# Kernel optimization log

Measured on AMD Instinct MI355X. Metric: run time of the kernel, lower is better.

Reference implementation:

```python
import jax, jax.numpy as jnp
import numpy as np


def _extract_patch_points(x, p):
    # x: (n, c, h, w) -> (n, c*p*p, h*w) patch feature vectors (edge-padded),
    # matching build_extended_map + build_pts_set_for_flann ordering.
    n, c, h, w = x.shape
    step = p // 2
    y = jnp.pad(x, ((0, 0), (0, 0), (step, step), (step, step)), mode='edge')
    shifts = [y[:, :, i:i + h, j:j + w] for i in range(p) for j in range(p)]
    feat = jnp.stack(shifts, axis=2)            # (n, c, p*p, h, w)
    return feat.reshape(n, c * p * p, h * w)    # (n, d, hw)


def setup_inputs() -> dict:
    key = jax.random.key(0)
    k1, k2 = jax.random.split(key)
    source_map = jax.random.normal(k1, (1, 32, 128, 128), dtype=jnp.float32)
    target_map = jax.random.normal(k2, (1, 32, 128, 128), dtype=jnp.float32)
    return {"source_map": source_map, "target_map": target_map, "patch_size": 3}


def reference(source_map, target_map, patch_size):
    n, c, sh, sw = source_map.shape
    tw = target_map.shape[3]
    pts = _extract_patch_points(target_map, patch_size)   # (n, d, Np)
    q_pts = _extract_patch_points(source_map, patch_size) # (n, d, Nq)

    def nn_one(p_feat, q_feat):
        p = p_feat.T  # (Np, d) target points
        q = q_feat.T  # (Nq, d) query points
        r_p = jnp.sum(p * p, axis=1, keepdims=True)   # (Np, 1)
        r_q = jnp.sum(q * q, axis=1, keepdims=True)   # (Nq, 1)
        mul = q @ p.T                                  # (Nq, Np)
        # Faithful to original pairwise_dist (its r_p/r_q broadcast orientation
        # requires Np == Nq, which holds here):
        dist = r_p - 2.0 * mul + r_q.T                 # (Nq, Np)
        return jnp.argmin(dist, axis=1), jnp.min(dist, axis=1)

    nn_idx, nnd = jax.vmap(nn_one)(pts, q_pts)         # (n, Nq) each
    idy = nn_idx // tw
    idx = nn_idx % tw
    nnf = jnp.stack([idy.reshape(n, sh, sw), idx.reshape(n, sh, sw)], axis=1).astype(jnp.int32)
    nnd = nnd.reshape(n, 1, sh, sw)
    return nnf, nnd
```

## Files before the change

### kernel.cpp

```cpp
#include <hip/hip_runtime.h>
#include <stdint.h>

#define NPT   16384
#define KE    64
#define ROWB  8192

typedef _Float16 f16;
typedef __attribute__((ext_vector_type(8))) _Float16 half8;
typedef __attribute__((ext_vector_type(4))) float floatx4;

#define AS1(p) ((const __attribute__((address_space(1))) uint32_t*)(p))
#define AS3(p) ((__attribute__((address_space(3))) uint32_t*)(p))

__global__ __launch_bounds__(256)
void extract_kernel(const float* __restrict__ src, const float* __restrict__ tgt,
                    f16* __restrict__ Aext, f16* __restrict__ Bext,
                    double* __restrict__ n2s, double* __restrict__ n2t) {
  __shared__ f16 bufA[256 * KE];
  __shared__ f16 bufB[256 * KE];
  const int tid = threadIdx.x;
  const int pt = blockIdx.x * 256 + tid;
  double sA = 0.0, sB = 0.0;
#pragma unroll
  for (int c = 0; c < 32; ++c) {
    float v = src[(c << 14) + pt];
    sA += (double)v * (double)v;
    f16 h = (f16)v;
    bufA[tid * KE + c] = h;
    bufA[tid * KE + 32 + c] = (f16)(v - (float)h);
    v = tgt[(c << 14) + pt];
    sB += (double)v * (double)v;
    h = (f16)v;
    bufB[tid * KE + c] = h;
    bufB[tid * KE + 32 + c] = (f16)(v - (float)h);
  }
  n2s[pt] = sA;
  n2t[pt] = sB;
  __syncthreads();
  const uint4* s4A = (const uint4*)bufA;
  const uint4* s4B = (const uint4*)bufB;
  uint4* gA = (uint4*)(Aext + (size_t)blockIdx.x * 256 * KE);
  uint4* gB = (uint4*)(Bext + (size_t)blockIdx.x * 256 * KE);
#pragma unroll
  for (int it = 0; it < 8; ++it) {
    gA[it * 256 + tid] = s4A[it * 256 + tid];
    gB[it * 256 + tid] = s4B[it * 256 + tid];
  }
}

__global__ __launch_bounds__(256)
void norm_blur_kernel(const double* __restrict__ n2s, const double* __restrict__ n2t,
                      float* __restrict__ rq, float* __restrict__ rp,
                      unsigned long long* __restrict__ best) {
  const int pt = blockIdx.x * 256 + threadIdx.x;
  const int y = pt >> 7, x = pt & 127;
  double sq = 0.0, sp_ = 0.0;
#pragma unroll
  for (int dy = -1; dy <= 1; ++dy) {
    int yy = y + dy; yy = yy < 0 ? 0 : (yy > 127 ? 127 : yy);
#pragma unroll
    for (int dx = -1; dx <= 1; ++dx) {
      int xx = x + dx; xx = xx < 0 ? 0 : (xx > 127 ? 127 : xx);
      sq  += n2s[(yy << 7) + xx];
      sp_ += n2t[(yy << 7) + xx];
    }
  }
  rq[pt] = (float)sq;
  rp[pt] = (float)sp_;
  best[pt] = 0xFFFFFFFFFFFFFFFFULL;
}

__global__ __launch_bounds__(256, 2)
void gemm_blur_argmin_kernel(const f16* __restrict__ A, const f16* __restrict__ B,
                             const float* __restrict__ rq,
                             unsigned long long* __restrict__ best) {
  __shared__ __align__(16) char smem[65536];
  f16* Ash = (f16*)smem;
  f16* Bsh = (f16*)(smem + 16384);
  float* Cf = (float*)smem;

  const int L  = blockIdx.x;
  const int st = L >> 7;
  const int r  = L & 127;
  const int bx = ((st & 15) << 3) | (r & 7);
  const int by = ((st >> 4) << 4) | (r >> 3);
  const int yq = by;
  const int vt = bx;

  const f16* Aw[3] = { A + (size_t)(yq > 0 ? yq - 1 : 0) * ROWB,
                       A + (size_t)yq * ROWB,
                       A + (size_t)(yq < 127 ? yq + 1 : 127) * ROWB };
  const f16* Bw[3] = { B + (size_t)(vt > 0 ? vt - 1 : 0) * ROWB,
                       B + (size_t)vt * ROWB,
                       B + (size_t)(vt < 127 ? vt + 1 : 127) * ROWB };

  const int t = threadIdx.x;
  const int w = t >> 6;
  const int l = t & 63;

  const int lr = l >> 3;
  const int lt = l & 7;
  const int sl = lt ^ (lr & 7);
  int rowOff[4];
#pragma unroll
  for (int ig = 0; ig < 4; ++ig)
    rowOff[ig] = (w * 32 + ig * 8 + lr) * KE + sl * 8;

  const int m16 = l & 15;
  const int q   = l >> 4;
  const int pHi = q ^ (m16 & 7);
  const int pLo = pHi ^ 4;
  const int wRow = (w & 1) * 64;
  const int wCol = (w >> 1) * 64;
  const int aHiOff = m16 * 64 + pHi * 8;
  const int aLoOff = m16 * 64 + pLo * 8;

  floatx4 acc[4][4] = {};

#pragma unroll
  for (int kw = 0; kw < 3; ++kw) {
    __syncthreads();
#pragma unroll
    for (int ig = 0; ig < 4; ++ig)
      __builtin_amdgcn_global_load_lds(AS1(Aw[kw] + rowOff[ig]),
                                       AS3(&Ash[(w * 32 + ig * 8) * 64]), 16, 0, 0);
#pragma unroll
    for (int ig = 0; ig < 4; ++ig)
      __builtin_amdgcn_global_load_lds(AS1(Bw[kw] + rowOff[ig]),
                                       AS3(&Bsh[(w * 32 + ig * 8) * 64]), 16, 0, 0);
    __syncthreads();

    half8 ah[4], al[4];
#pragma unroll
    for (int i = 0; i < 4; ++i) {
      ah[i] = *(const half8*)&Ash[(wRow + i * 16) * 64 + aHiOff];
      al[i] = *(const half8*)&Ash[(wRow + i * 16) * 64 + aLoOff];
    }
#pragma unroll
    for (int j = 0; j < 4; ++j) {
      half8 bh = *(const half8*)&Bsh[(wCol + j * 16) * 64 + aHiOff];
#pragma unroll
      for (int i = 0; i < 4; ++i)
        acc[i][j] = __builtin_amdgcn_mfma_f32_16x16x32_f16(ah[i], bh, acc[i][j], 0, 0, 0);
#pragma unroll
      for (int i = 0; i < 4; ++i)
        acc[i][j] = __builtin_amdgcn_mfma_f32_16x16x32_f16(al[i], bh, acc[i][j], 0, 0, 0);
    }
#pragma unroll
    for (int j = 0; j < 4; ++j) {
      half8 bl = *(const half8*)&Bsh[(wCol + j * 16) * 64 + aLoOff];
#pragma unroll
      for (int i = 0; i < 4; ++i)
        acc[i][j] = __builtin_amdgcn_mfma_f32_16x16x32_f16(ah[i], bl, acc[i][j], 0, 0, 0);
    }
  }

  __syncthreads();
#pragma unroll
  for (int i = 0; i < 4; ++i) {
#pragma unroll
    for (int j = 0; j < 4; ++j) {
      const int col = wCol + j * 16 + m16;
      const int gc = col >> 2, cl = col & 3;
#pragma unroll
      for (int r2 = 0; r2 < 4; ++r2) {
        const int rr = wRow + i * 16 + q * 4 + r2;
        Cf[(rr << 7) + (((gc ^ (rr & 7)) << 2) | cl)] = acc[i][j][r2];
      }
    }
  }
  __syncthreads();

  const int xr = t >> 1;
  const int uh = t & 1;
  const int g0 = uh << 4;
  const int xm = xr > 0 ? xr - 1 : 0;
  const int xp = xr < 127 ? xr + 1 : 127;

  const floatx4* rq4 = (const floatx4*)(rq + (vt << 7));

#define LDCF(x, g) (*(const floatx4*)&Cf[((x) << 7) + ((((g) ^ ((x) & 7))) << 2)])

  unsigned long long pk = 0xFFFFFFFFFFFFFFFFULL;
  float am_last = (uh == 0) ? LDCF(xm, 0)[0] : LDCF(xm, 15)[3];
  floatx4 Ap = LDCF(xp, g0);
#pragma unroll
  for (int k = 0; k < 16; ++k) {
    const int g = g0 + k;
    const floatx4 Am = LDCF(xm, g);
    const floatx4 Ac = LDCF(xr, g);
    floatx4 ApN = Ap;
    float ap4;
    if (g < 31) { ApN = LDCF(xp, g + 1); ap4 = ApN[0]; }
    else        { ap4 = Ap[3]; }
    const floatx4 rv = rq4[g];
    float o[4];
    o[0] = am_last + Ac[0] + Ap[1];
    o[1] = Am[0]   + Ac[1] + Ap[2];
    o[2] = Am[1]   + Ac[2] + Ap[3];
    o[3] = Am[2]   + Ac[3] + ap4;
    am_last = Am[3];
    Ap = ApN;
    const int colb = (vt << 7) + (g << 2);
#pragma unroll
    for (int e = 0; e < 4; ++e) {
      float f = fmaf(-2.0f, o[e], rv[e]);
      unsigned int bits = __float_as_uint(f);
      unsigned int key = (bits & 0x80000000u) ? ~bits : (bits | 0x80000000u);
      unsigned long long cand =
          ((unsigned long long)key << 32) | (unsigned)(colb + e);
      pk = pk < cand ? pk : cand;
    }
  }
  unsigned long long ov = __shfl_xor(pk, 1);
  pk = pk < ov ? pk : ov;
  if (uh == 0) atomicMin(best + (yq << 7) + xr, pk);
}

__global__ void finalize_kernel(const unsigned long long* __restrict__ best,
                                const float* __restrict__ rp,
                                float* __restrict__ out) {
  int i = blockIdx.x * 256 + threadIdx.x;
  if (i >= NPT) return;
  unsigned long long v = best[i];
  unsigned int col = (unsigned int)(v & 0xFFFFFFFFu);
  unsigned int key = (unsigned int)(v >> 32);
  unsigned int bits = (key & 0x80000000u) ? (key & 0x7FFFFFFFu) : ~key;
  float fmin = __uint_as_float(bits);
  out[i]           = (float)(col >> 7);
  out[NPT + i]     = (float)(col & 127);
  out[2 * NPT + i] = rp[i] + fmin;
}

extern "C" void kernel_launch(void* const* d_in, const int* in_sizes, int n_in,
                              void* d_out, int out_size, void* d_ws, size_t ws_size,
                              hipStream_t stream) {
  const float* src = (const float*)d_in[0];
  const float* tgt = (const float*)d_in[1];
  float* out = (float*)d_out;

  char* ws = (char*)d_ws;
  f16* Aext = (f16*)(ws);
  f16* Bext = (f16*)(ws + 2097152);
  double* n2s = (double*)(ws + 4194304);
  double* n2t = (double*)(ws + 4325376);
  float* rq = (float*)(ws + 4456448);
  float* rp = (float*)(ws + 4521984);
  unsigned long long* best = (unsigned long long*)(ws + 4587520);

  extract_kernel<<<64, 256, 0, stream>>>(src, tgt, Aext, Bext, n2s, n2t);
  norm_blur_kernel<<<64, 256, 0, stream>>>(n2s, n2t, rq, rp, best);
  gemm_blur_argmin_kernel<<<16384, 256, 0, stream>>>(Aext, Bext, rq, best);
  finalize_kernel<<<NPT / 256, 256, 0, stream>>>(best, rp, out);
}
```

Measured before the change: 344.4 us.

## Load GEMM operands directly to registers and halve epilogue LDS for higher occupancy

The GEMM stage now loads A/B fragments straight from global memory into registers instead of staging them through LDS with global_load_lds. The epilogue writes the 128x128 C tile to a 65-row LDS buffer in two phases, with a halo row, which cuts shared memory from 64KB to about 33KB. Launch bounds are raised to 4 blocks per CU. The argmin now tracks a float/index pair instead of packed 64-bit keys, with 4 threads per row. The cost is uncoalesced direct global fragment loads and an extra barrier phase.

```diff
diff --git a/kernel.cpp b/kernel.cpp
--- a/kernel.cpp
+++ b/kernel.cpp
@@ -8,9 +8,6 @@
 typedef _Float16 f16;
 typedef __attribute__((ext_vector_type(8))) _Float16 half8;
 typedef __attribute__((ext_vector_type(4))) float floatx4;
-
-#define AS1(p) ((const __attribute__((address_space(1))) uint32_t*)(p))
-#define AS3(p) ((__attribute__((address_space(3))) uint32_t*)(p))
 
 __global__ __launch_bounds__(256)
 void extract_kernel(const float* __restrict__ src, const float* __restrict__ tgt,
@@ -70,14 +67,11 @@
   best[pt] = 0xFFFFFFFFFFFFFFFFULL;
 }
 
-__global__ __launch_bounds__(256, 2)
+__global__ __launch_bounds__(256, 4)
 void gemm_blur_argmin_kernel(const f16* __restrict__ A, const f16* __restrict__ B,
                              const float* __restrict__ rq,
                              unsigned long long* __restrict__ best) {
-  __shared__ __align__(16) char smem[65536];
-  f16* Ash = (f16*)smem;
-  f16* Bsh = (f16*)(smem + 16384);
-  float* Cf = (float*)smem;
+  __shared__ __align__(16) float Cf[65 * 128];
 
   const int L  = blockIdx.x;
   const int st = L >> 7;
@@ -97,124 +91,124 @@
   const int t = threadIdx.x;
   const int w = t >> 6;
   const int l = t & 63;
-
-  const int lr = l >> 3;
-  const int lt = l & 7;
-  const int sl = lt ^ (lr & 7);
-  int rowOff[4];
-#pragma unroll
-  for (int ig = 0; ig < 4; ++ig)
-    rowOff[ig] = (w * 32 + ig * 8 + lr) * KE + sl * 8;
-
   const int m16 = l & 15;
   const int q   = l >> 4;
-  const int pHi = q ^ (m16 & 7);
-  const int pLo = pHi ^ 4;
   const int wRow = (w & 1) * 64;
   const int wCol = (w >> 1) * 64;
-  const int aHiOff = m16 * 64 + pHi * 8;
-  const int aLoOff = m16 * 64 + pLo * 8;
+
+  int aIdx[4], bIdx[4];
+#pragma unroll
+  for (int i = 0; i < 4; ++i) aIdx[i] = (wRow + i * 16 + m16) * KE + q * 8;
+#pragma unroll
+  for (int j = 0; j < 4; ++j) bIdx[j] = (wCol + j * 16 + m16) * KE + q * 8;
 
   floatx4 acc[4][4] = {};
 
 #pragma unroll
   for (int kw = 0; kw < 3; ++kw) {
+    const f16* __restrict__ Ak = Aw[kw];
+    const f16* __restrict__ Bk = Bw[kw];
+    half8 ah[4], al[4], bh[4], bl[4];
+#pragma unroll
+    for (int i = 0; i < 4; ++i) {
+      ah[i] = *(const half8*)(Ak + aIdx[i]);
+      al[i] = *(const half8*)(Ak + aIdx[i] + 32);
+    }
+#pragma unroll
+    for (int j = 0; j < 4; ++j) {
+      bh[j] = *(const half8*)(Bk + bIdx[j]);
+      bl[j] = *(const half8*)(Bk + bIdx[j] + 32);
+    }
+#pragma unroll
+    for (int j = 0; j < 4; ++j) {
+#pragma unroll
+      for (int i = 0; i < 4; ++i)
+        acc[i][j] = __builtin_amdgcn_mfma_f32_16x16x32_f16(ah[i], bh[j], acc[i][j], 0, 0, 0);
+#pragma unroll
+      for (int i = 0; i < 4; ++i)
+        acc[i][j] = __builtin_amdgcn_mfma_f32_16x16x32_f16(al[i], bh[j], acc[i][j], 0, 0, 0);
+#pragma unroll
+      for (int i = 0; i < 4; ++i)
+        acc[i][j] = __builtin_amdgcn_mfma_f32_16x16x32_f16(ah[i], bl[j], acc[i][j], 0, 0, 0);
+    }
+  }
+
+#define SWZ(row, col) (((row) << 7) + ((((col) >> 2) ^ ((row) & 7)) << 2) + ((col) & 3))
+#define LDCF(row, g) (*(const floatx4*)&Cf[((row) << 7) + ((((g) ^ ((row) & 7))) << 2)])
+
+  const int xr_l = t >> 2;
+  const int uq = t & 3;
+  const int g0 = uq << 3;
+  const floatx4* rq4 = (const floatx4*)(rq + (vt << 7));
+
+#pragma unroll
+  for (int ph = 0; ph < 2; ++ph) {
+    if ((ph == 0) ? (wRow == 0) : (wRow == 64)) {
+      const int rbase = ph;
+#pragma unroll
+      for (int i = 0; i < 4; ++i)
+#pragma unroll
+        for (int j = 0; j < 4; ++j) {
+          const int col = wCol + j * 16 + m16;
+#pragma unroll
+          for (int r2 = 0; r2 < 4; ++r2) {
+            const int lrow = rbase + i * 16 + q * 4 + r2;
+            Cf[SWZ(lrow, col)] = acc[i][j][r2];
+          }
+        }
+    } else if ((ph == 0) ? (q == 0) : (q == 3)) {
+      const int lrow = ph ? 0 : 64;
+#pragma unroll
+      for (int j = 0; j < 4; ++j) {
+        const int col = wCol + j * 16 + m16;
+        Cf[SWZ(lrow, col)] = ph ? acc[3][j][3] : acc[0][j][0];
+      }
+    }
     __syncthreads();
-#pragma unroll
-    for (int ig = 0; ig < 4; ++ig)
-      __builtin_amdgcn_global_load_lds(AS1(Aw[kw] + rowOff[ig]),
-                                       AS3(&Ash[(w * 32 + ig * 8) * 64]), 16, 0, 0);
-#pragma unroll
-    for (int ig = 0; ig < 4; ++ig)
-      __builtin_amdgcn_global_load_lds(AS1(Bw[kw] + rowOff[ig]),
-                                       AS3(&Bsh[(w * 32 + ig * 8) * 64]), 16, 0, 0);
-    __syncthreads();
-
-    half8 ah[4], al[4];
-#pragma unroll
-    for (int i = 0; i < 4; ++i) {
-      ah[i] = *(const half8*)&Ash[(wRow + i * 16) * 64 + aHiOff];
-      al[i] = *(const half8*)&Ash[(wRow + i * 16) * 64 + aLoOff];
-    }
-#pragma unroll
-    for (int j = 0; j < 4; ++j) {
-      half8 bh = *(const half8*)&Bsh[(wCol + j * 16) * 64 + aHiOff];
-#pragma unroll
-      for (int i = 0; i < 4; ++i)
-        acc[i][j] = __builtin_amdgcn_mfma_f32_16x16x32_f16(ah[i], bh, acc[i][j], 0, 0, 0);
-#pragma unroll
-      for (int i = 0; i < 4; ++i)
-        acc[i][j] = __builtin_amdgcn_mfma_f32_16x16x32_f16(al[i], bh, acc[i][j], 0, 0, 0);
-    }
-#pragma unroll
-    for (int j = 0; j < 4; ++j) {
-      half8 bl = *(const half8*)&Bsh[(wCol + j * 16) * 64 + aLoOff];
-#pragma unroll
-      for (int i = 0; i < 4; ++i)
-        acc[i][j] = __builtin_amdgcn_mfma_f32_16x16x32_f16(ah[i], bl, acc[i][j], 0, 0, 0);
-    }
-  }
-
-  __syncthreads();
-#pragma unroll
-  for (int i = 0; i < 4; ++i) {
-#pragma unroll
-    for (int j = 0; j < 4; ++j) {
-      const int col = wCol + j * 16 + m16;
-      const int gc = col >> 2, cl = col & 3;
-#pragma unroll
-      for (int r2 = 0; r2 < 4; ++r2) {
-        const int rr = wRow + i * 16 + q * 4 + r2;
-        Cf[(rr << 7) + (((gc ^ (rr & 7)) << 2) | cl)] = acc[i][j][r2];
-      }
-    }
-  }
-  __syncthreads();
-
-  const int xr = t >> 1;
-  const int uh = t & 1;
-  const int g0 = uh << 4;
-  const int xm = xr > 0 ? xr - 1 : 0;
-  const int xp = xr < 127 ? xr + 1 : 127;
-
-  const floatx4* rq4 = (const floatx4*)(rq + (vt << 7));
-
-#define LDCF(x, g) (*(const floatx4*)&Cf[((x) << 7) + ((((g) ^ ((x) & 7))) << 2)])
-
-  unsigned long long pk = 0xFFFFFFFFFFFFFFFFULL;
-  float am_last = (uh == 0) ? LDCF(xm, 0)[0] : LDCF(xm, 15)[3];
-  floatx4 Ap = LDCF(xp, g0);
-#pragma unroll
-  for (int k = 0; k < 16; ++k) {
-    const int g = g0 + k;
-    const floatx4 Am = LDCF(xm, g);
-    const floatx4 Ac = LDCF(xr, g);
-    floatx4 ApN = Ap;
-    float ap4;
-    if (g < 31) { ApN = LDCF(xp, g + 1); ap4 = ApN[0]; }
-    else        { ap4 = Ap[3]; }
-    const floatx4 rv = rq4[g];
-    float o[4];
-    o[0] = am_last + Ac[0] + Ap[1];
-    o[1] = Am[0]   + Ac[1] + Ap[2];
-    o[2] = Am[1]   + Ac[2] + Ap[3];
-    o[3] = Am[2]   + Ac[3] + ap4;
-    am_last = Am[3];
-    Ap = ApN;
-    const int colb = (vt << 7) + (g << 2);
-#pragma unroll
-    for (int e = 0; e < 4; ++e) {
-      float f = fmaf(-2.0f, o[e], rv[e]);
-      unsigned int bits = __float_as_uint(f);
-      unsigned int key = (bits & 0x80000000u) ? ~bits : (bits | 0x80000000u);
-      unsigned long long cand =
-          ((unsigned long long)key << 32) | (unsigned)(colb + e);
-      pk = pk < cand ? pk : cand;
-    }
-  }
-  unsigned long long ov = __shfl_xor(pk, 1);
-  pk = pk < ov ? pk : ov;
-  if (uh == 0) atomicMin(best + (yq << 7) + xr, pk);
+
+    const int x   = ph * 64 + xr_l;
+    const int lx  = ph ? xr_l + 1 : xr_l;
+    const int lxm = ph ? lx - 1 : (xr_l ? xr_l - 1 : 0);
+    const int lxp = (ph && x == 127) ? lx : lx + 1;
+
+    float bf = __builtin_huge_valf();
+    int bu = 0;
+    float am_last = (uq == 0) ? LDCF(lxm, 0)[0] : LDCF(lxm, g0 - 1)[3];
+    floatx4 Ap = LDCF(lxp, g0);
+#pragma unroll
+    for (int k = 0; k < 8; ++k) {
+      const int g = g0 + k;
+      const floatx4 Am = LDCF(lxm, g);
+      const floatx4 Ac = LDCF(lx, g);
+      floatx4 ApN = Ap;
+      float ap4;
+      if (k < 7)       { ApN = LDCF(lxp, g + 1); ap4 = ApN[0]; }
+      else if (uq < 3) { ap4 = LDCF(lxp, g + 1)[0]; }
+      else             { ap4 = Ap[3]; }
+      const floatx4 rv = rq4[g];
+      float o0 = am_last + Ac[0] + Ap[1];
+      float o1 = Am[0]   + Ac[1] + Ap[2];
+      float o2 = Am[1]   + Ac[2] + Ap[3];
+      float o3 = Am[2]   + Ac[3] + ap4;
+      am_last = Am[3];
+      Ap = ApN;
+      const int ub = g << 2;
+      float f0 = fmaf(-2.0f, o0, rv[0]); if (f0 < bf) { bf = f0; bu = ub; }
+      float f1 = fmaf(-2.0f, o1, rv[1]); if (f1 < bf) { bf = f1; bu = ub + 1; }
+      float f2 = fmaf(-2.0f, o2, rv[2]); if (f2 < bf) { bf = f2; bu = ub + 2; }
+      float f3 = fmaf(-2.0f, o3, rv[3]); if (f3 < bf) { bf = f3; bu = ub + 3; }
+    }
+    unsigned int bits = __float_as_uint(bf);
+    unsigned int key = (bits & 0x80000000u) ? ~bits : (bits | 0x80000000u);
+    unsigned long long pk =
+        ((unsigned long long)key << 32) | (unsigned)((vt << 7) + bu);
+    unsigned long long o1v = __shfl_xor(pk, 1); pk = pk < o1v ? pk : o1v;
+    unsigned long long o2v = __shfl_xor(pk, 2); pk = pk < o2v ? pk : o2v;
+    if (uq == 0) atomicMin(best + (yq << 7) + x, pk);
+    if (ph == 0) __syncthreads();
+  }
+#undef SWZ
+#undef LDCF
 }
 
 __global__ void finalize_kernel(const unsigned long long* __restrict__ best,
```

Result: slower. 1.007 ms (+192.5%).
